# Kernel tuning notes

Hardware: AMD Instinct MI355X
Metric: run time of the kernel (lower is better)

## Reference

```python
import jax, jax.numpy as jnp
import numpy as np

V, E, H, L, B, T = 32000, 512, 512, 2, 16, 128


def setup_inputs() -> dict:
    key = jax.random.key(0)
    ks = jax.random.split(key, 12)
    s = 0.05  # small init to keep gates in a sane range
    return {
        "embedding": jax.random.normal(ks[0], (V, E), jnp.float32),
        "h": jax.random.normal(ks[1], (L, B, H), jnp.float32),
        "c": jax.random.normal(ks[2], (L, B, H), jnp.float32),
        "encoder_outputs": jax.random.normal(ks[3], (T, B, H), jnp.float32),
        # LSTM layer 0: input_size = H + E
        "w_ih0": jax.random.normal(ks[4], (4 * H, H + E), jnp.float32) * s,
        "w_hh0": jax.random.normal(ks[5], (4 * H, H), jnp.float32) * s,
        "b_ih0": jnp.zeros((4 * H,), jnp.float32),
        "b_hh0": jnp.zeros((4 * H,), jnp.float32),
        # LSTM layer 1: input_size = H
        "w_ih1": jax.random.normal(ks[6], (4 * H, H), jnp.float32) * s,
        "w_hh1": jax.random.normal(ks[7], (4 * H, H), jnp.float32) * s,
        "b_ih1": jnp.zeros((4 * H,), jnp.float32),
        "b_hh1": jnp.zeros((4 * H,), jnp.float32),
        # output projection to vocab
        "out_w": jax.random.normal(ks[8], (V, H), jnp.float32) * s,
        "out_b": jnp.zeros((V,), jnp.float32),
    }


def reference(embedding, h, c, encoder_outputs,
              w_ih0, w_hh0, b_ih0, b_hh0,
              w_ih1, w_hh1, b_ih1, b_hh1,
              out_w, out_b):
    T_, B_, _ = encoder_outputs.shape

    def cell(x, hp, cp, wi, wh, bi, bh):
        # PyTorch LSTM gate order: i, f, g, o
        g = x @ wi.T + hp @ wh.T + (bi + bh)
        i, f, gg, o = jnp.split(g, 4, axis=-1)
        cn = jax.nn.sigmoid(f) * cp + jax.nn.sigmoid(i) * jnp.tanh(gg)
        hn = jax.nn.sigmoid(o) * jnp.tanh(cn)
        return hn, cn

    def step(carry, _):
        tok, hs, cs = carry          # tok: [B] int, hs/cs: [L,B,H]
        emb = embedding[tok]         # [B,E] pretrained-embedding lookup
        # dot attention: query = top LSTM layer hidden state
        scores = jnp.einsum('bh,sbh->bs', hs[-1], encoder_outputs)
        aw = jax.nn.softmax(scores, axis=-1)               # [B,S]
        ctx = jnp.einsum('bs,sbh->bh', aw, encoder_outputs)  # [B,H]
        x = jnp.concatenate([emb, ctx], axis=-1)           # [B,E+H]
        h0, c0 = cell(x, hs[0], cs[0], w_ih0, w_hh0, b_ih0, b_hh0)
        h1, c1 = cell(h0, hs[1], cs[1], w_ih1, w_hh1, b_ih1, b_hh1)
        logp = jax.nn.log_softmax(h1 @ out_w.T + out_b, axis=-1)  # [B,V]
        nxt = jnp.argmax(logp, axis=-1).astype(jnp.int32)  # greedy (topk(1))
        return (nxt, jnp.stack([h0, h1]), jnp.stack([c0, c1])), (logp, nxt, aw)

    tok0 = jnp.ones((B_,), jnp.int32)  # torch.ones(batch_size) start token
    _, (logp, seq, attn) = jax.lax.scan(step, (tok0, h, c), None, length=T_)
    # torch cats along dim=1 -> [B, T, ...]
    return (jnp.transpose(logp, (1, 0, 2)),
            jnp.transpose(seq, (1, 0)),
            jnp.transpose(attn, (1, 0, 2)))
```

## Files before the change

### kernel.cpp

```cpp
#include <hip/hip_runtime.h>
#include <math.h>

#define VV 32000
#define EE 512
#define HH 512
#define BB 16
#define TT 128
#define SS 128
#define XD 1024
#define NPB 500
#define VB 64
#define SROW 1728

__device__ __forceinline__ float sigf(float x) { return 1.0f / (1.0f + expf(-x)); }

__global__ __launch_bounds__(256) void k_proj(
    const float* __restrict__ out_w, const float* __restrict__ out_b,
    const float* __restrict__ h1,
    const float* __restrict__ enc,
    float* __restrict__ raw, long rawstride, int nt_raw,
    float* __restrict__ scores,
    float* __restrict__ pmax, float* __restrict__ psum, int* __restrict__ pidx,
    int npb, int do_scores)
{
    const int blk = blockIdx.x;
    const int tid = threadIdx.x;

    if (blk >= npb) {
        if (!do_scores) return;
        const int b = blk - npb;
        const int s = tid >> 1, h = tid & 1;
        const float* er = enc + ((long)s * BB + b) * HH + h * 256;
        const float* hh = h1 + b * HH + h * 256;
        float acc = 0.f;
        #pragma unroll 8
        for (int k = 0; k < 256; k += 4) {
            float4 w = *(const float4*)(er + k);
            float4 x = *(const float4*)(hh + k);
            acc += w.x * x.x + w.y * x.y + w.z * x.z + w.w * x.w;
        }
        acc += __shfl_xor(acc, 1);
        if (h == 0) scores[b * SS + s] = acc;
        return;
    }

    __shared__ float h1t[10304];
    __shared__ float lv[64][17];

    for (int i = tid; i < BB * HH; i += 256) {
        int b = i >> 9, k = i & 511;
        h1t[k * 20 + ((k >> 6) << 2) + b] = h1[i];
    }
    __syncthreads();

    const int q = tid >> 3;
    const int h = tid & 7;
    const int v = blk * VB + q * 2;
    const float* w0 = out_w + (long)v * HH;
    const float* w1 = w0 + HH;
    float acc0[16], acc1[16];
    #pragma unroll
    for (int i = 0; i < 16; ++i) { acc0[i] = 0.f; acc1[i] = 0.f; }

    const int kbase = h * 64;
    for (int kk = 0; kk < 64; kk += 4) {
        const int k = kbase + kk;
        float a0f[4], a1f[4];
        *(float4*)a0f = *(const float4*)(w0 + k);
        *(float4*)a1f = *(const float4*)(w1 + k);
        #pragma unroll
        for (int d = 0; d < 4; ++d) {
            const int kd = k + d;
            const float* hp = &h1t[kd * 20 + ((kd >> 6) << 2)];
            const float wA = a0f[d], wB = a1f[d];
            #pragma unroll
            for (int g = 0; g < 4; ++g) {
                float hvf[4];
                *(float4*)hvf = *(const float4*)(hp + g * 4);
                acc0[g*4+0] += wA * hvf[0]; acc0[g*4+1] += wA * hvf[1];
                acc0[g*4+2] += wA * hvf[2]; acc0[g*4+3] += wA * hvf[3];
                acc1[g*4+0] += wB * hvf[0]; acc1[g*4+1] += wB * hvf[1];
                acc1[g*4+2] += wB * hvf[2]; acc1[g*4+3] += wB * hvf[3];
            }
        }
    }
    #pragma unroll
    for (int i = 0; i < 16; ++i) {
        float a = acc0[i];
        a += __shfl_xor(a, 1); a += __shfl_xor(a, 2); a += __shfl_xor(a, 4);
        acc0[i] = a;
        float c = acc1[i];
        c += __shfl_xor(c, 1); c += __shfl_xor(c, 2); c += __shfl_xor(c, 4);
        acc1[i] = c;
    }
    if (h == 0) {
        const float b0 = out_b[v], b1 = out_b[v + 1];
        #pragma unroll
        for (int b = 0; b < 16; ++b) {
            const float l0 = acc0[b] + b0, l1 = acc1[b] + b1;
            lv[q * 2][b] = l0; lv[q * 2 + 1][b] = l1;
            float* dst = raw + (long)b * rawstride + v;
            if (nt_raw) {
                __builtin_nontemporal_store(l0, dst);
                __builtin_nontemporal_store(l1, dst + 1);
            } else {
                dst[0] = l0; dst[1] = l1;
            }
        }
    }
    __syncthreads();

    const int b2 = tid >> 4;
    const int l  = tid & 15;
    float vals[4];
    float m = -INFINITY; int mi = 0;
    #pragma unroll
    for (int r = 0; r < 4; ++r) {
        const float x = lv[l * 4 + r][b2];
        vals[r] = x;
        if (x > m) { m = x; mi = l * 4 + r; }
    }
    #pragma unroll
    for (int off = 8; off >= 1; off >>= 1) {
        const float om = __shfl_xor(m, off);
        const int   oi = __shfl_xor(mi, off);
        if (om > m || (om == m && oi < mi)) { m = om; mi = oi; }
    }
    float z = 0.f;
    #pragma unroll
    for (int r = 0; r < 4; ++r) z += expf(vals[r] - m);
    #pragma unroll
    for (int off = 8; off >= 1; off >>= 1) z += __shfl_xor(z, off);
    if (l == 0) {
        pmax[blk * 16 + b2] = m;
        psum[blk * 16 + b2] = z;
        pidx[blk * 16 + b2] = blk * VB + mi;
    }
}

__global__ __launch_bounds__(256) void k_prep(
    const float* __restrict__ embedding,
    const float* __restrict__ enc,
    const float* __restrict__ scores,
    const float* __restrict__ raw, long rawstride, int nt_raw,
    const float* __restrict__ pmax, const float* __restrict__ psum, const int* __restrict__ pidx,
    float* __restrict__ xout,
    float* __restrict__ logp_out, float* __restrict__ seq_out, float* __restrict__ attn_out,
    int t, int mode, int npb)
{
    const int b = blockIdx.x >> 4;
    const int chunk = blockIdx.x & 15;
    const int tid = threadIdx.x;

    __shared__ float sm[256]; __shared__ int si[256]; __shared__ float ssum[256];
    __shared__ float aw[SS];  __shared__ float sred[2];

    int tok = 1;
    if (mode & 1) {
        float m = -INFINITY; int mi = 0x7fffffff;
        for (int i = tid; i < npb; i += 256) {
            const float pm = pmax[i * 16 + b];
            const int   pi = pidx[i * 16 + b];
            if (pm > m || (pm == m && pi < mi)) { m = pm; mi = pi; }
        }
        sm[tid] = m; si[tid] = mi;
        __syncthreads();
        for (int o = 128; o > 0; o >>= 1) {
            if (tid < o) {
                const float om = sm[tid + o]; const int oi = si[tid + o];
                if (om > sm[tid] || (om == sm[tid] && oi < si[tid])) { sm[tid] = om; si[tid] = oi; }
            }
            __syncthreads();
        }
        const float M = sm[0]; tok = si[0];
        float z = 0.f;
        for (int i = tid; i < npb; i += 256)
            z += psum[i * 16 + b] * expf(pmax[i * 16 + b] - M);
        ssum[tid] = z;
        __syncthreads();
        for (int o = 128; o > 0; o >>= 1) {
            if (tid < o) ssum[tid] += ssum[tid + o];
            __syncthreads();
        }
        const float lse = M + logf(ssum[0]);

        const float* rb = raw + (long)b * rawstride + chunk * 2000;
        float* ob = logp_out + ((long)b * TT + (t - 1)) * VV + chunk * 2000;
        if (nt_raw) {
            for (int i = tid; i < 2000; i += 256)
                __builtin_nontemporal_store(__builtin_nontemporal_load(rb + i) - lse, ob + i);
        } else {
            for (int i = tid; i < 2000; i += 256)
                __builtin_nontemporal_store(rb[i] - lse, ob + i);
        }
        if (chunk == 0 && tid == 0)
            __builtin_nontemporal_store((float)tok, seq_out + b * TT + (t - 1));
    }
    if (!(mode & 2)) return;
    __syncthreads();

    if (tid == 0) {
        float mm = -INFINITY;
        for (int s = 0; s < SS; ++s) mm = fmaxf(mm, scores[b * SS + s]);
        sred[0] = mm;
    }
    __syncthreads();
    if (tid < SS) aw[tid] = expf(scores[b * SS + tid] - sred[0]);
    __syncthreads();
    if (tid == 0) {
        float sum = 0.f;
        for (int s = 0; s < SS; ++s) sum += aw[s];
        sred[1] = 1.0f / sum;
    }
    __syncthreads();
    if (tid < SS) aw[tid] *= sred[1];
    __syncthreads();
    if (chunk == 0 && tid < SS)
        __builtin_nontemporal_store(aw[tid], attn_out + ((long)b * TT + t) * SS + tid);

    const int e0 = chunk * 64;
    if (e0 < EE) {
        for (int i = tid; i < 64; i += 256)
            xout[b * XD + e0 + i] = embedding[(long)tok * EE + e0 + i];
    } else {
        const int h0 = e0 - EE;
        __shared__ float ps[4][64];
        const int o = tid & 63, part = tid >> 6;
        float a = 0.f;
        for (int s2 = part * 32; s2 < part * 32 + 32; ++s2)
            a += aw[s2] * enc[((long)s2 * BB + b) * HH + h0 + o];
        ps[part][o] = a;
        __syncthreads();
        if (tid < 64)
            xout[b * XD + e0 + tid] = ps[0][tid] + ps[1][tid] + ps[2][tid] + ps[3][tid];
    }
}

__global__ __launch_bounds__(256) void k_lstm(
    const float* __restrict__ wih, const float* __restrict__ whh,
    const float* __restrict__ bih, const float* __restrict__ bhh,
    const float* __restrict__ xin, int xlen, int xshift,
    const float* __restrict__ hprev, const float* __restrict__ cprev,
    float* __restrict__ hout, float* __restrict__ cout)
{
    __shared__ float xs[BB * SROW];
    __shared__ float gpart[8 * 16 * 17];

    const int tid = threadIdx.x;
    const int j0 = blockIdx.x * 2;
    const int tot = xlen + HH;

    const int xmask = xlen - 1;
    for (int i = tid; i < (BB << xshift); i += 256) {
        const int b = i >> xshift, k = i & xmask;
        xs[b * SROW + k + ((k >> 5) << 2)] = xin[i];
    }
    for (int i = tid; i < BB * HH; i += 256) {
        const int b = i >> 9, k = xlen + (i & 511);
        xs[b * SROW + k + ((k >> 5) << 2)] = hprev[i];
    }
    __syncthreads();

    const int b = tid >> 4;
    const int h = tid & 15;
    const int klen = tot >> 4;
    const int k0 = h * klen;

    const float* pih[8]; const float* phh[8];
    #pragma unroll
    for (int r = 0; r < 8; ++r) {
        const int g = r >> 1, jj = r & 1;
        const int row = g * HH + j0 + jj;
        pih[r] = wih + (long)row * xlen;
        phh[r] = whh + (long)row * HH - xlen;
    }
    float acc[8];
    #pragma unroll
    for (int r = 0; r < 8; ++r) acc[r] = 0.f;

    const float* xb = xs + b * SROW;
    #pragma unroll 4
    for (int i = 0; i < klen; i += 4) {
        const int k = k0 + i;
        float xvf[4];
        *(float4*)xvf = *(const float4*)(xb + k + ((k >> 5) << 2));
        #pragma unroll
        for (int r = 0; r < 8; ++r) {
            const float* wp = ((k < xlen) ? pih[r] : phh[r]) + k;
            float wvf[4];
            *(float4*)wvf = *(const float4*)wp;
            acc[r] += wvf[0]*xvf[0] + wvf[1]*xvf[1] + wvf[2]*xvf[2] + wvf[3]*xvf[3];
        }
    }
    #pragma unroll
    for (int r = 0; r < 8; ++r) gpart[(r * 16 + b) * 17 + h] = acc[r];
    __syncthreads();

    if (tid < 128) {
        const int r = tid >> 4, bb = tid & 15;
        float s = 0.f;
        #pragma unroll
        for (int hh2 = 0; hh2 < 16; ++hh2) s += gpart[(r * 16 + bb) * 17 + hh2];
        const int g = r >> 1, jj = r & 1;
        const int row = g * HH + j0 + jj;
        gpart[(r * 16 + bb) * 17 + 16] = s + bih[row] + bhh[row];
    }
    __syncthreads();

    if (tid < 32) {
        const int bb = tid >> 1, jj = tid & 1;
        const float ii = gpart[((0 + jj) * 16 + bb) * 17 + 16];
        const float ff = gpart[((2 + jj) * 16 + bb) * 17 + 16];
        const float gg = gpart[((4 + jj) * 16 + bb) * 17 + 16];
        const float oo = gpart[((6 + jj) * 16 + bb) * 17 + 16];
        const int j = j0 + jj;
        const float cp = cprev[bb * HH + j];
        const float cn = sigf(ff) * cp + sigf(ii) * tanhf(gg);
        const float hn = sigf(oo) * tanhf(cn);
        hout[bb * HH + j] = hn;
        cout[bb * HH + j] = cn;
    }
}

extern "C" void kernel_launch(void* const* d_in, const int* in_sizes, int n_in,
                              void* d_out, int out_size, void* d_ws, size_t ws_size,
                              hipStream_t stream)
{
    (void)in_sizes; (void)n_in; (void)out_size;

    const float* embedding = (const float*)d_in[0];
    const float* h_in  = (const float*)d_in[1];
    const float* c_in  = (const float*)d_in[2];
    const float* enc   = (const float*)d_in[3];
    const float* w_ih0 = (const float*)d_in[4];
    const float* w_hh0 = (const float*)d_in[5];
    const float* b_ih0 = (const float*)d_in[6];
    const float* b_hh0 = (const float*)d_in[7];
    const float* w_ih1 = (const float*)d_in[8];
    const float* w_hh1 = (const float*)d_in[9];
    const float* b_ih1 = (const float*)d_in[10];
    const float* b_hh1 = (const float*)d_in[11];
    const float* out_w = (const float*)d_in[12];
    const float* out_b = (const float*)d_in[13];

    float* out = (float*)d_out;
    const long logp_sz = (long)BB * TT * VV;
    const long seq_sz  = (long)BB * TT;
    float* seq_out  = out + logp_sz;
    float* attn_out = out + logp_sz + seq_sz;

    float* ws = (float*)d_ws;
    const int BH = BB * HH;
    float* st     = ws;
    float* xbuf   = st + 8 * BH;
    float* scores = xbuf + BB * XD;
    float* pm     = scores + BB * SS;
    float* psm    = pm + NPB * BB;
    int*   pid    = (int*)(psm + NPB * BB);
    float* lraw   = (float*)(pid + NPB * BB);
    const size_t need = (size_t)((char*)(lraw + (long)BB * VV) - (char*)ws);
    const int usews = (ws_size >= need) ? 1 : 0;
    const int nt_raw = usews ? 0 : 1;
    const long rawstride = usews ? (long)VV : (long)TT * VV;

    auto sbuf = [&](int buf, int slot) { return st + (size_t)(buf * 4 + slot) * BH; };

    k_proj<<<16, 256, 0, stream>>>(out_w, out_b, h_in + BH, enc,
                                   usews ? lraw : out, rawstride, nt_raw,
                                   scores, pm, psm, pid, 0, 1);

    for (int t = 0; t <= TT; ++t) {
        const int mode = (t > 0 ? 1 : 0) | (t < TT ? 2 : 0);
        const float* rawprev = usews ? lraw : out + (size_t)(t > 0 ? t - 1 : 0) * VV;
        k_prep<<<256, 256, 0, stream>>>(embedding, enc, scores,
                                        rawprev, rawstride, nt_raw,
                                        pm, psm, pid, xbuf,
                                        out, seq_out, attn_out, t, mode, NPB);
        if (t == TT) break;

        const float* h0c = t ? sbuf(t & 1, 0) : h_in;
        const float* c0c = t ? sbuf(t & 1, 1) : c_in;
        const float* h1c = t ? sbuf(t & 1, 2) : h_in + BH;
        const float* c1c = t ? sbuf(t & 1, 3) : c_in + BH;
        const int n = (t + 1) & 1;
        float* h0n = sbuf(n, 0); float* c0n = sbuf(n, 1);
        float* h1n = sbuf(n, 2); float* c1n = sbuf(n, 3);

        k_lstm<<<256, 256, 0, stream>>>(w_ih0, w_hh0, b_ih0, b_hh0,
                                        xbuf, 1024, 10, h0c, c0c, h0n, c0n);
        k_lstm<<<256, 256, 0, stream>>>(w_ih1, w_hh1, b_ih1, b_hh1,
                                        h0n, 512, 9, h1c, c1c, h1n, c1n);

        float* rawt = usews ? lraw : out + (size_t)t * VV;
        k_proj<<<NPB + 16, 256, 0, stream>>>(out_w, out_b, h1n, enc,
                                             rawt, rawstride, nt_raw,
                                             scores, pm, psm, pid, NPB, 1);
    }
}
```

Before: 13.02 ms.

## Fuse decode loop into one persistent cooperative kernel with grid syncs

Replaces the per-timestep launches of prep, two LSTM and projection kernels with a single cooperative kernel that loops over all timesteps and separates stages with grid-wide syncs. The vocab projection is retiled to 128 rows per 512-thread block with a register reduce-scatter, and the attention, context and log-softmax finalisation stages are redistributed across blocks. The aim is to remove hundreds of kernel launch gaps and the per-launch reload of small state. In exchange it depends on cooperative launch residency (256 blocks of 512 threads) and pays the latency of four grid barriers per step.

```diff
diff --git a/kernel.cpp b/kernel.cpp
--- a/kernel.cpp
+++ b/kernel.cpp
@@ -1,5 +1,8 @@
 #include <hip/hip_runtime.h>
+#include <hip/hip_cooperative_groups.h>
 #include <math.h>
+
+namespace cg = cooperative_groups;
 
 #define VV 32000
 #define EE 512
@@ -8,317 +11,347 @@
 #define TT 128
 #define SS 128
 #define XD 1024
-#define NPB 500
-#define VB 64
-#define SROW 1728
-
-__device__ __forceinline__ float sigf(float x) { return 1.0f / (1.0f + expf(-x)); }
-
-__global__ __launch_bounds__(256) void k_proj(
-    const float* __restrict__ out_w, const float* __restrict__ out_b,
-    const float* __restrict__ h1,
-    const float* __restrict__ enc,
-    float* __restrict__ raw, long rawstride, int nt_raw,
-    float* __restrict__ scores,
-    float* __restrict__ pmax, float* __restrict__ psum, int* __restrict__ pidx,
-    int npb, int do_scores)
-{
+#define NPB 250
+#define BH (BB*HH)
+
+__device__ __forceinline__ float sigf(float x){ return 1.0f/(1.0f+expf(-x)); }
+
+__device__ __forceinline__ float fget(const float4& v, int d){
+    return d==0 ? v.x : d==1 ? v.y : d==2 ? v.z : v.w;
+}
+
+__device__ __forceinline__ int lvoff(int row){ return row * 20 + (((row >> 2) & 1) << 2); }
+
+__device__ __forceinline__ float bredmax(float v, float* s8, int tid){
+    #pragma unroll
+    for (int o = 32; o >= 1; o >>= 1) v = fmaxf(v, __shfl_xor(v, o));
+    if ((tid & 63) == 0) s8[tid >> 6] = v;
+    __syncthreads();
+    float r = fmaxf(fmaxf(fmaxf(s8[0],s8[1]),fmaxf(s8[2],s8[3])),
+                    fmaxf(fmaxf(s8[4],s8[5]),fmaxf(s8[6],s8[7])));
+    __syncthreads();
+    return r;
+}
+__device__ __forceinline__ float bredsum(float v, float* s8, int tid){
+    #pragma unroll
+    for (int o = 32; o >= 1; o >>= 1) v += __shfl_xor(v, o);
+    if ((tid & 63) == 0) s8[tid >> 6] = v;
+    __syncthreads();
+    float r = ((s8[0]+s8[1])+(s8[2]+s8[3]))+((s8[4]+s8[5])+(s8[6]+s8[7]));
+    __syncthreads();
+    return r;
+}
+__device__ __forceinline__ void bredamax(float& v, int& idx, float* s8, int* si8, int tid){
+    #pragma unroll
+    for (int o = 32; o >= 1; o >>= 1){
+        float ov = __shfl_xor(v, o); int oi = __shfl_xor(idx, o);
+        if (ov > v || (ov == v && oi < idx)) { v = ov; idx = oi; }
+    }
+    if ((tid & 63) == 0) { s8[tid >> 6] = v; si8[tid >> 6] = idx; }
+    __syncthreads();
+    float bv = s8[0]; int bi = si8[0];
+    #pragma unroll
+    for (int w = 1; w < 8; ++w){
+        float ov = s8[w]; int oi = si8[w];
+        if (ov > bv || (ov == bv && oi < bi)) { bv = ov; bi = oi; }
+    }
+    __syncthreads();
+    v = bv; idx = bi;
+}
+
+template<int XLEN>
+__device__ __forceinline__ void lstm_cell(
+    int tid, int j0,
+    const float* __restrict__ wih, const float* __restrict__ whh,
+    const float* __restrict__ bih, const float* __restrict__ bhh,
+    const float* __restrict__ xsrc,
+    const float* __restrict__ hold, const float* __restrict__ cold,
+    float* __restrict__ hnew, float* __restrict__ cnew)
+{
+    const int bb = tid >> 5, h32 = tid & 31;
+    constexpr int KX = XLEN >> 5;
+    constexpr int KH = 16;
+    float acc[8];
+    #pragma unroll
+    for (int r = 0; r < 8; ++r) acc[r] = 0.f;
+    const float* xb = xsrc + bb * XLEN + h32 * KX;
+    const float* hb = hold + (bb << 9) + h32 * KH;
+    const float* wx[8]; const float* wh[8];
+    #pragma unroll
+    for (int r = 0; r < 8; ++r) {
+        const int row = (r >> 1) * HH + j0 + (r & 1);
+        wx[r] = wih + (long)row * XLEN + h32 * KX;
+        wh[r] = whh + ((long)row << 9) + h32 * KH;
+    }
+    #pragma unroll
+    for (int i = 0; i < KX; i += 4) {
+        float4 xv = *(const float4*)(xb + i);
+        #pragma unroll
+        for (int r = 0; r < 8; ++r) {
+            float4 wv = *(const float4*)(wx[r] + i);
+            acc[r] = fmaf(wv.w, xv.w, fmaf(wv.z, xv.z, fmaf(wv.y, xv.y, fmaf(wv.x, xv.x, acc[r]))));
+        }
+    }
+    #pragma unroll
+    for (int i = 0; i < KH; i += 4) {
+        float4 xv = *(const float4*)(hb + i);
+        #pragma unroll
+        for (int r = 0; r < 8; ++r) {
+            float4 wv = *(const float4*)(wh[r] + i);
+            acc[r] = fmaf(wv.w, xv.w, fmaf(wv.z, xv.z, fmaf(wv.y, xv.y, fmaf(wv.x, xv.x, acc[r]))));
+        }
+    }
+    #pragma unroll
+    for (int o = 16; o >= 1; o >>= 1) {
+        #pragma unroll
+        for (int r = 0; r < 8; ++r) acc[r] += __shfl_xor(acc[r], o);
+    }
+    if (h32 == 0) {
+        #pragma unroll
+        for (int jj = 0; jj < 2; ++jj) {
+            const int j = j0 + jj;
+            const float gi = acc[0 + jj] + bih[j]          + bhh[j];
+            const float gf = acc[2 + jj] + bih[HH + j]     + bhh[HH + j];
+            const float gg = acc[4 + jj] + bih[2*HH + j]   + bhh[2*HH + j];
+            const float go = acc[6 + jj] + bih[3*HH + j]   + bhh[3*HH + j];
+            const float cp = cold[(bb << 9) + j];
+            const float cn = sigf(gf) * cp + sigf(gi) * tanhf(gg);
+            const float hn = sigf(go) * tanhf(cn);
+            hnew[(bb << 9) + j] = hn;
+            cnew[(bb << 9) + j] = cn;
+        }
+    }
+}
+
+__device__ __forceinline__ void calc_scores(int blk, int tid,
+    const float* __restrict__ h1, const float* __restrict__ enc, float* __restrict__ scores)
+{
+    const int idx = (blk - NPB) * 512 + tid;
+    if (idx >= BB * SS) return;
+    const int s = idx >> 4, b = idx & 15;
+    const float* ep = enc + ((long)s * BB + b) * HH;
+    const float* hp = h1 + b * HH;
+    float a0 = 0.f, a1 = 0.f, a2 = 0.f, a3 = 0.f;
+    #pragma unroll 2
+    for (int k = 0; k < HH; k += 16) {
+        float4 e0 = *(const float4*)(ep + k),      hv0 = *(const float4*)(hp + k);
+        float4 e1 = *(const float4*)(ep + k + 4),  hv1 = *(const float4*)(hp + k + 4);
+        float4 e2 = *(const float4*)(ep + k + 8),  hv2 = *(const float4*)(hp + k + 8);
+        float4 e3 = *(const float4*)(ep + k + 12), hv3 = *(const float4*)(hp + k + 12);
+        a0 += e0.x*hv0.x + e0.y*hv0.y + e0.z*hv0.z + e0.w*hv0.w;
+        a1 += e1.x*hv1.x + e1.y*hv1.y + e1.z*hv1.z + e1.w*hv1.w;
+        a2 += e2.x*hv2.x + e2.y*hv2.y + e2.z*hv2.z + e2.w*hv2.w;
+        a3 += e3.x*hv3.x + e3.y*hv3.y + e3.z*hv3.z + e3.w*hv3.w;
+    }
+    scores[b * SS + s] = (a0 + a1) + (a2 + a3);
+}
+
+__device__ __forceinline__ void proj_tile(
+    int blk, int tid, const float* __restrict__ h1,
+    const float* __restrict__ ow, const float* __restrict__ ob,
+    float* __restrict__ rawt, long rstride,
+    float* __restrict__ pm, float* __restrict__ psm, int* __restrict__ pid,
+    float* __restrict__ h1t, float* __restrict__ lv)
+{
+    for (int i = tid; i < BB * HH; i += 512) {
+        const int b = i >> 9, k = i & 511;
+        h1t[k * 20 + ((k >> 5) << 2) + b] = h1[i];
+    }
+    __syncthreads();
+
+    const int q = tid >> 4, h = tid & 15;
+    const int v0 = blk * 128 + q * 4;
+    const int k0 = h << 5;
+    float a[64];
+    #pragma unroll
+    for (int i = 0; i < 64; ++i) a[i] = 0.f;
+
+    const float* w0 = ow + (long)v0 * HH + k0;
+    #pragma unroll 2
+    for (int kk = 0; kk < 32; kk += 4) {
+        float4 wv0 = *(const float4*)(w0 + kk);
+        float4 wv1 = *(const float4*)(w0 + HH + kk);
+        float4 wv2 = *(const float4*)(w0 + 2 * HH + kk);
+        float4 wv3 = *(const float4*)(w0 + 3 * HH + kk);
+        #pragma unroll
+        for (int d = 0; d < 4; ++d) {
+            const int kd = k0 + kk + d;
+            const float* hp = h1t + kd * 20 + ((kd >> 5) << 2);
+            float4 hv0 = *(const float4*)(hp);
+            float4 hv1 = *(const float4*)(hp + 4);
+            float4 hv2 = *(const float4*)(hp + 8);
+            float4 hv3 = *(const float4*)(hp + 12);
+            const float hv[16] = {hv0.x,hv0.y,hv0.z,hv0.w, hv1.x,hv1.y,hv1.z,hv1.w,
+                                  hv2.x,hv2.y,hv2.z,hv2.w, hv3.x,hv3.y,hv3.z,hv3.w};
+            const float wr[4] = { fget(wv0,d), fget(wv1,d), fget(wv2,d), fget(wv3,d) };
+            #pragma unroll
+            for (int r = 0; r < 4; ++r)
+                #pragma unroll
+                for (int j = 0; j < 16; ++j)
+                    a[r*16+j] = fmaf(wr[r], hv[j], a[r*16+j]);
+        }
+    }
+
+#define RS_ROUND(O, NH)                                                  \
+    {                                                                    \
+        const bool up = (h & (O)) != 0;                                  \
+        _Pragma("unroll")                                                \
+        for (int i = 0; i < (NH); ++i) {                                 \
+            float lo = a[i], hi = a[i + (NH)];                           \
+            float snd = up ? lo : hi;                                    \
+            float rcv = __shfl_xor(snd, (O));                            \
+            a[i] = (up ? hi : lo) + rcv;                                 \
+        }                                                                \
+    }
+    RS_ROUND(1, 32)
+    RS_ROUND(2, 16)
+    RS_ROUND(4, 8)
+    RS_ROUND(8, 4)
+#undef RS_ROUND
+    const int br = ((h & 1) << 3) | ((h & 2) << 1) | ((h & 4) >> 1) | ((h & 8) >> 3);
+    const int rr = br >> 2;
+    const int jb = (br & 3) << 2;
+    {
+        const int row = q * 4 + rr;
+        const float bv = ob[v0 + rr];
+        float* dst = lv + lvoff(row) + jb;
+        float4 val = { a[0] + bv, a[1] + bv, a[2] + bv, a[3] + bv };
+        *(float4*)dst = val;
+    }
+    __syncthreads();
+
+    for (int i = tid; i < 128 * BB; i += 512) {
+        const int b = i >> 7, row = i & 127;
+        rawt[(long)b * rstride + blk * 128 + row] = lv[lvoff(row) + b];
+    }
+
+    const int b2 = tid >> 5, l = tid & 31;
+    float vals[4]; float m = -INFINITY; int mi = 0;
+    #pragma unroll
+    for (int r = 0; r < 4; ++r) {
+        const int row = l * 4 + r;
+        const float x = lv[lvoff(row) + b2];
+        vals[r] = x;
+        if (x > m) { m = x; mi = row; }
+    }
+    #pragma unroll
+    for (int o = 16; o >= 1; o >>= 1) {
+        float om = __shfl_xor(m, o); int oi = __shfl_xor(mi, o);
+        if (om > m || (om == m && oi < mi)) { m = om; mi = oi; }
+    }
+    float z = 0.f;
+    #pragma unroll
+    for (int r = 0; r < 4; ++r) z += expf(vals[r] - m);
+    #pragma unroll
+    for (int o = 16; o >= 1; o >>= 1) z += __shfl_xor(z, o);
+    if (l == 0) {
+        pm[blk * BB + b2] = m;
+        psm[blk * BB + b2] = z;
+        pid[blk * BB + b2] = blk * 128 + mi;
+    }
+}
+
+struct Params {
+    const float *emb, *h0i, *c0i, *enc;
+    const float *wih0, *whh0, *bih0, *bhh0;
+    const float *wih1, *whh1, *bih1, *bhh1;
+    const float *ow, *ob;
+    float *out, *seqo, *attn;
+    float *st, *xbuf, *scores, *pm, *psm;
+    int *pid;
+    float *lraw;
+    int usews;
+};
+
+__global__ __launch_bounds__(512, 2) void k_decode(Params p)
+{
+    cg::grid_group grid = cg::this_grid();
     const int blk = blockIdx.x;
     const int tid = threadIdx.x;
 
-    if (blk >= npb) {
-        if (!do_scores) return;
-        const int b = blk - npb;
-        const int s = tid >> 1, h = tid & 1;
-        const float* er = enc + ((long)s * BB + b) * HH + h * 256;
-        const float* hh = h1 + b * HH + h * 256;
-        float acc = 0.f;
-        #pragma unroll 8
-        for (int k = 0; k < 256; k += 4) {
-            float4 w = *(const float4*)(er + k);
-            float4 x = *(const float4*)(hh + k);
-            acc += w.x * x.x + w.y * x.y + w.z * x.z + w.w * x.w;
-        }
-        acc += __shfl_xor(acc, 1);
-        if (h == 0) scores[b * SS + s] = acc;
-        return;
-    }
-
-    __shared__ float h1t[10304];
-    __shared__ float lv[64][17];
-
-    for (int i = tid; i < BB * HH; i += 256) {
-        int b = i >> 9, k = i & 511;
-        h1t[k * 20 + ((k >> 6) << 2) + b] = h1[i];
-    }
-    __syncthreads();
-
-    const int q = tid >> 3;
-    const int h = tid & 7;
-    const int v = blk * VB + q * 2;
-    const float* w0 = out_w + (long)v * HH;
-    const float* w1 = w0 + HH;
-    float acc0[16], acc1[16];
-    #pragma unroll
-    for (int i = 0; i < 16; ++i) { acc0[i] = 0.f; acc1[i] = 0.f; }
-
-    const int kbase = h * 64;
-    for (int kk = 0; kk < 64; kk += 4) {
-        const int k = kbase + kk;
-        float a0f[4], a1f[4];
-        *(float4*)a0f = *(const float4*)(w0 + k);
-        *(float4*)a1f = *(const float4*)(w1 + k);
-        #pragma unroll
-        for (int d = 0; d < 4; ++d) {
-            const int kd = k + d;
-            const float* hp = &h1t[kd * 20 + ((kd >> 6) << 2)];
-            const float wA = a0f[d], wB = a1f[d];
-            #pragma unroll
-            for (int g = 0; g < 4; ++g) {
-                float hvf[4];
-                *(float4*)hvf = *(const float4*)(hp + g * 4);
-                acc0[g*4+0] += wA * hvf[0]; acc0[g*4+1] += wA * hvf[1];
-                acc0[g*4+2] += wA * hvf[2]; acc0[g*4+3] += wA * hvf[3];
-                acc1[g*4+0] += wB * hvf[0]; acc1[g*4+1] += wB * hvf[1];
-                acc1[g*4+2] += wB * hvf[2]; acc1[g*4+3] += wB * hvf[3];
+    __shared__ float smem[12896];
+    float* h1t = smem;
+    float* lv  = smem + 10304;
+    float* aw  = smem;
+    float* s8  = smem + 160;
+    int*   si8 = (int*)(smem + 176);
+
+    if (blk >= NPB) calc_scores(blk, tid, p.h0i + BH, p.enc, p.scores);
+    grid.sync();
+
+    for (int t = 0; t <= TT; ++t) {
+        if (blk < BB) {
+            const int b = blk;
+            int tok = 1;
+            if (t > 0) {
+                float m = -INFINITY; int mi = 0x7fffffff;
+                if (tid < NPB) { m = p.pm[tid * BB + b]; mi = p.pid[tid * BB + b]; }
+                bredamax(m, mi, s8, si8, tid);
+                tok = mi;
+                if (tid == 0) p.seqo[b * TT + (t - 1)] = (float)tok;
             }
-        }
-    }
-    #pragma unroll
-    for (int i = 0; i < 16; ++i) {
-        float a = acc0[i];
-        a += __shfl_xor(a, 1); a += __shfl_xor(a, 2); a += __shfl_xor(a, 4);
-        acc0[i] = a;
-        float c = acc1[i];
-        c += __shfl_xor(c, 1); c += __shfl_xor(c, 2); c += __shfl_xor(c, 4);
-        acc1[i] = c;
-    }
-    if (h == 0) {
-        const float b0 = out_b[v], b1 = out_b[v + 1];
-        #pragma unroll
-        for (int b = 0; b < 16; ++b) {
-            const float l0 = acc0[b] + b0, l1 = acc1[b] + b1;
-            lv[q * 2][b] = l0; lv[q * 2 + 1][b] = l1;
-            float* dst = raw + (long)b * rawstride + v;
-            if (nt_raw) {
-                __builtin_nontemporal_store(l0, dst);
-                __builtin_nontemporal_store(l1, dst + 1);
-            } else {
-                dst[0] = l0; dst[1] = l1;
+            if (t < TT) {
+                float sc = (tid < SS) ? p.scores[b * SS + tid] : -INFINITY;
+                float M = bredmax(sc, s8, tid);
+                float e = (tid < SS) ? expf(sc - M) : 0.f;
+                float Z = bredsum(e, s8, tid);
+                float av = e / Z;
+                if (tid < SS) {
+                    aw[tid] = av;
+                    __builtin_nontemporal_store(av, p.attn + ((long)b * TT + t) * SS + tid);
+                }
+                __syncthreads();
+                float cacc = 0.f;
+                const float* ep = p.enc + b * HH + tid;
+                #pragma unroll 8
+                for (int s = 0; s < SS; ++s)
+                    cacc = fmaf(aw[s], ep[(long)s * BH], cacc);
+                p.xbuf[b * XD + EE + tid] = cacc;
+                p.xbuf[b * XD + tid] = p.emb[(long)tok * EE + tid];
             }
-        }
-    }
-    __syncthreads();
-
-    const int b2 = tid >> 4;
-    const int l  = tid & 15;
-    float vals[4];
-    float m = -INFINITY; int mi = 0;
-    #pragma unroll
-    for (int r = 0; r < 4; ++r) {
-        const float x = lv[l * 4 + r][b2];
-        vals[r] = x;
-        if (x > m) { m = x; mi = l * 4 + r; }
-    }
-    #pragma unroll
-    for (int off = 8; off >= 1; off >>= 1) {
-        const float om = __shfl_xor(m, off);
-        const int   oi = __shfl_xor(mi, off);
-        if (om > m || (om == m && oi < mi)) { m = om; mi = oi; }
-    }
-    float z = 0.f;
-    #pragma unroll
-    for (int r = 0; r < 4; ++r) z += expf(vals[r] - m);
-    #pragma unroll
-    for (int off = 8; off >= 1; off >>= 1) z += __shfl_xor(z, off);
-    if (l == 0) {
-        pmax[blk * 16 + b2] = m;
-        psum[blk * 16 + b2] = z;
-        pidx[blk * 16 + b2] = blk * VB + mi;
-    }
-}
-
-__global__ __launch_bounds__(256) void k_prep(
-    const float* __restrict__ embedding,
-    const float* __restrict__ enc,
-    const float* __restrict__ scores,
-    const float* __restrict__ raw, long rawstride, int nt_raw,
-    const float* __restrict__ pmax, const float* __restrict__ psum, const int* __restrict__ pidx,
-    float* __restrict__ xout,
-    float* __restrict__ logp_out, float* __restrict__ seq_out, float* __restrict__ attn_out,
-    int t, int mode, int npb)
-{
-    const int b = blockIdx.x >> 4;
-    const int chunk = blockIdx.x & 15;
-    const int tid = threadIdx.x;
-
-    __shared__ float sm[256]; __shared__ int si[256]; __shared__ float ssum[256];
-    __shared__ float aw[SS];  __shared__ float sred[2];
-
-    int tok = 1;
-    if (mode & 1) {
-        float m = -INFINITY; int mi = 0x7fffffff;
-        for (int i = tid; i < npb; i += 256) {
-            const float pm = pmax[i * 16 + b];
-            const int   pi = pidx[i * 16 + b];
-            if (pm > m || (pm == m && pi < mi)) { m = pm; mi = pi; }
-        }
-        sm[tid] = m; si[tid] = mi;
-        __syncthreads();
-        for (int o = 128; o > 0; o >>= 1) {
-            if (tid < o) {
-                const float om = sm[tid + o]; const int oi = si[tid + o];
-                if (om > sm[tid] || (om == sm[tid] && oi < si[tid])) { sm[tid] = om; si[tid] = oi; }
-            }
-            __syncthreads();
-        }
-        const float M = sm[0]; tok = si[0];
-        float z = 0.f;
-        for (int i = tid; i < npb; i += 256)
-            z += psum[i * 16 + b] * expf(pmax[i * 16 + b] - M);
-        ssum[tid] = z;
-        __syncthreads();
-        for (int o = 128; o > 0; o >>= 1) {
-            if (tid < o) ssum[tid] += ssum[tid + o];
-            __syncthreads();
-        }
-        const float lse = M + logf(ssum[0]);
-
-        const float* rb = raw + (long)b * rawstride + chunk * 2000;
-        float* ob = logp_out + ((long)b * TT + (t - 1)) * VV + chunk * 2000;
-        if (nt_raw) {
-            for (int i = tid; i < 2000; i += 256)
-                __builtin_nontemporal_store(__builtin_nontemporal_load(rb + i) - lse, ob + i);
-        } else {
-            for (int i = tid; i < 2000; i += 256)
-                __builtin_nontemporal_store(rb[i] - lse, ob + i);
-        }
-        if (chunk == 0 && tid == 0)
-            __builtin_nontemporal_store((float)tok, seq_out + b * TT + (t - 1));
-    }
-    if (!(mode & 2)) return;
-    __syncthreads();
-
-    if (tid == 0) {
-        float mm = -INFINITY;
-        for (int s = 0; s < SS; ++s) mm = fmaxf(mm, scores[b * SS + s]);
-        sred[0] = mm;
-    }
-    __syncthreads();
-    if (tid < SS) aw[tid] = expf(scores[b * SS + tid] - sred[0]);
-    __syncthreads();
-    if (tid == 0) {
-        float sum = 0.f;
-        for (int s = 0; s < SS; ++s) sum += aw[s];
-        sred[1] = 1.0f / sum;
-    }
-    __syncthreads();
-    if (tid < SS) aw[tid] *= sred[1];
-    __syncthreads();
-    if (chunk == 0 && tid < SS)
-        __builtin_nontemporal_store(aw[tid], attn_out + ((long)b * TT + t) * SS + tid);
-
-    const int e0 = chunk * 64;
-    if (e0 < EE) {
-        for (int i = tid; i < 64; i += 256)
-            xout[b * XD + e0 + i] = embedding[(long)tok * EE + e0 + i];
-    } else {
-        const int h0 = e0 - EE;
-        __shared__ float ps[4][64];
-        const int o = tid & 63, part = tid >> 6;
-        float a = 0.f;
-        for (int s2 = part * 32; s2 < part * 32 + 32; ++s2)
-            a += aw[s2] * enc[((long)s2 * BB + b) * HH + h0 + o];
-        ps[part][o] = a;
-        __syncthreads();
-        if (tid < 64)
-            xout[b * XD + e0 + tid] = ps[0][tid] + ps[1][tid] + ps[2][tid] + ps[3][tid];
-    }
-}
-
-__global__ __launch_bounds__(256) void k_lstm(
-    const float* __restrict__ wih, const float* __restrict__ whh,
-    const float* __restrict__ bih, const float* __restrict__ bhh,
-    const float* __restrict__ xin, int xlen, int xshift,
-    const float* __restrict__ hprev, const float* __restrict__ cprev,
-    float* __restrict__ hout, float* __restrict__ cout)
-{
-    __shared__ float xs[BB * SROW];
-    __shared__ float gpart[8 * 16 * 17];
-
-    const int tid = threadIdx.x;
-    const int j0 = blockIdx.x * 2;
-    const int tot = xlen + HH;
-
-    const int xmask = xlen - 1;
-    for (int i = tid; i < (BB << xshift); i += 256) {
-        const int b = i >> xshift, k = i & xmask;
-        xs[b * SROW + k + ((k >> 5) << 2)] = xin[i];
-    }
-    for (int i = tid; i < BB * HH; i += 256) {
-        const int b = i >> 9, k = xlen + (i & 511);
-        xs[b * SROW + k + ((k >> 5) << 2)] = hprev[i];
-    }
-    __syncthreads();
-
-    const int b = tid >> 4;
-    const int h = tid & 15;
-    const int klen = tot >> 4;
-    const int k0 = h * klen;
-
-    const float* pih[8]; const float* phh[8];
-    #pragma unroll
-    for (int r = 0; r < 8; ++r) {
-        const int g = r >> 1, jj = r & 1;
-        const int row = g * HH + j0 + jj;
-        pih[r] = wih + (long)row * xlen;
-        phh[r] = whh + (long)row * HH - xlen;
-    }
-    float acc[8];
-    #pragma unroll
-    for (int r = 0; r < 8; ++r) acc[r] = 0.f;
-
-    const float* xb = xs + b * SROW;
-    #pragma unroll 4
-    for (int i = 0; i < klen; i += 4) {
-        const int k = k0 + i;
-        float xvf[4];
-        *(float4*)xvf = *(const float4*)(xb + k + ((k >> 5) << 2));
-        #pragma unroll
-        for (int r = 0; r < 8; ++r) {
-            const float* wp = ((k < xlen) ? pih[r] : phh[r]) + k;
-            float wvf[4];
-            *(float4*)wvf = *(const float4*)wp;
-            acc[r] += wvf[0]*xvf[0] + wvf[1]*xvf[1] + wvf[2]*xvf[2] + wvf[3]*xvf[3];
-        }
-    }
-    #pragma unroll
-    for (int r = 0; r < 8; ++r) gpart[(r * 16 + b) * 17 + h] = acc[r];
-    __syncthreads();
-
-    if (tid < 128) {
-        const int r = tid >> 4, bb = tid & 15;
-        float s = 0.f;
-        #pragma unroll
-        for (int hh2 = 0; hh2 < 16; ++hh2) s += gpart[(r * 16 + bb) * 17 + hh2];
-        const int g = r >> 1, jj = r & 1;
-        const int row = g * HH + j0 + jj;
-        gpart[(r * 16 + bb) * 17 + 16] = s + bih[row] + bhh[row];
-    }
-    __syncthreads();
-
-    if (tid < 32) {
-        const int bb = tid >> 1, jj = tid & 1;
-        const float ii = gpart[((0 + jj) * 16 + bb) * 17 + 16];
-        const float ff = gpart[((2 + jj) * 16 + bb) * 17 + 16];
-        const float gg = gpart[((4 + jj) * 16 + bb) * 17 + 16];
-        const float oo = gpart[((6 + jj) * 16 + bb) * 17 + 16];
-        const int j = j0 + jj;
-        const float cp = cprev[bb * HH + j];
-        const float cn = sigf(ff) * cp + sigf(ii) * tanhf(gg);
-        const float hn = sigf(oo) * tanhf(cn);
-        hout[bb * HH + j] = hn;
-        cout[bb * HH + j] = cn;
+        } else if (t > 0) {
+            const int wb = blk - BB;
+            const int b = wb / 15, c = wb - b * 15;
+            float m = (tid < NPB) ? p.pm[tid * BB + b] : -INFINITY;
+            m = bredmax(m, s8, tid);
+            float z = (tid < NPB) ? p.psm[tid * BB + b] * expf(p.pm[tid * BB + b] - m) : 0.f;
+            z = bredsum(z, s8, tid);
+            const float lse = m + logf(z);
+            const long obase = ((long)b * TT + (t - 1)) * (long)VV;
+            const float* rb = p.usews ? (p.lraw + (long)b * VV) : (p.out + obase);
+            float* obp = p.out + obase;
+            const int v0 = c * 2134, v1 = min(v0 + 2134, VV);
+            for (int v = v0 + tid; v < v1; v += 512)
+                __builtin_nontemporal_store(__builtin_nontemporal_load(rb + v) - lse, obp + v);
+        }
+        if (t == TT) return;
+        grid.sync();
+
+        const int po = t & 1, pn = (t + 1) & 1;
+        const float* h0o = t ? p.st + (po * 4 + 0) * BH : p.h0i;
+        const float* c0o = t ? p.st + (po * 4 + 1) * BH : p.c0i;
+        const float* h1o = t ? p.st + (po * 4 + 2) * BH : p.h0i + BH;
+        const float* c1o = t ? p.st + (po * 4 + 3) * BH : p.c0i + BH;
+        float* h0n = p.st + (pn * 4 + 0) * BH;
+        float* c0n = p.st + (pn * 4 + 1) * BH;
+        float* h1n = p.st + (pn * 4 + 2) * BH;
+        float* c1n = p.st + (pn * 4 + 3) * BH;
+
+        lstm_cell<XD>(tid, blk * 2, p.wih0, p.whh0, p.bih0, p.bhh0, p.xbuf, h0o, c0o, h0n, c0n);
+        grid.sync();
+
+        lstm_cell<HH>(tid, blk * 2, p.wih1, p.whh1, p.bih1, p.bhh1, h0n, h1o, c1o, h1n, c1n);
+        grid.sync();
+
+        {
+            float* rawt = p.usews ? p.lraw : p.out + (long)t * VV;
+            const long rstride = p.usews ? (long)VV : (long)TT * (long)VV;
+            if (blk < NPB)
+                proj_tile(blk, tid, h1n, p.ow, p.ob, rawt, rstride, p.pm, p.psm, p.pid, h1t, lv);
+            else
+                calc_scores(blk, tid, h1n, p.enc, p.scores);
+        }
+        grid.sync();
     }
 }
 
@@ -327,73 +360,38 @@
                               hipStream_t stream)
 {
     (void)in_sizes; (void)n_in; (void)out_size;
-
-    const float* embedding = (const float*)d_in[0];
-    const float* h_in  = (const float*)d_in[1];
-    const float* c_in  = (const float*)d_in[2];
-    const float* enc   = (const float*)d_in[3];
-    const float* w_ih0 = (const float*)d_in[4];
-    const float* w_hh0 = (const float*)d_in[5];
-    const float* b_ih0 = (const float*)d_in[6];
-    const float* b_hh0 = (const float*)d_in[7];
-    const float* w_ih1 = (const float*)d_in[8];
-    const float* w_hh1 = (const float*)d_in[9];
-    const float* b_ih1 = (const float*)d_in[10];
-    const float* b_hh1 = (const float*)d_in[11];
-    const float* out_w = (const float*)d_in[12];
-    const float* out_b = (const float*)d_in[13];
+    Params p;
+    p.emb  = (const float*)d_in[0];
+    p.h0i  = (const float*)d_in[1];
+    p.c0i  = (const float*)d_in[2];
+    p.enc  = (const float*)d_in[3];
+    p.wih0 = (const float*)d_in[4];
+    p.whh0 = (const float*)d_in[5];
+    p.bih0 = (const float*)d_in[6];
+    p.bhh0 = (const float*)d_in[7];
+    p.wih1 = (const float*)d_in[8];
+    p.whh1 = (const float*)d_in[9];
+    p.bih1 = (const float*)d_in[10];
+    p.bhh1 = (const float*)d_in[11];
+    p.ow   = (const float*)d_in[12];
+    p.ob   = (const float*)d_in[13];
 
     float* out = (float*)d_out;
-    const long logp_sz = (long)BB * TT * VV;
-    const long seq_sz  = (long)BB * TT;
-    float* seq_out  = out + logp_sz;
-    float* attn_out = out + logp_sz + seq_sz;
+    p.out  = out;
+    p.seqo = out + (long)BB * TT * VV;
+    p.attn = p.seqo + (long)BB * TT;
 
     float* ws = (float*)d_ws;
-    const int BH = BB * HH;
-    float* st     = ws;
-    float* xbuf   = st + 8 * BH;
-    float* scores = xbuf + BB * XD;
-    float* pm     = scores + BB * SS;
-    float* psm    = pm + NPB * BB;
-    int*   pid    = (int*)(psm + NPB * BB);
-    float* lraw   = (float*)(pid + NPB * BB);
-    const size_t need = (size_t)((char*)(lraw + (long)BB * VV) - (char*)ws);
-    const int usews = (ws_size >= need) ? 1 : 0;
-    const int nt_raw = usews ? 0 : 1;
-    const long rawstride = usews ? (long)VV : (long)TT * VV;
-
-    auto sbuf = [&](int buf, int slot) { return st + (size_t)(buf * 4 + slot) * BH; };
-
-    k_proj<<<16, 256, 0, stream>>>(out_w, out_b, h_in + BH, enc,
-                                   usews ? lraw : out, rawstride, nt_raw,
-                                   scores, pm, psm, pid, 0, 1);
-
-    for (int t = 0; t <= TT; ++t) {
-        const int mode = (t > 0 ? 1 : 0) | (t < TT ? 2 : 0);
-        const float* rawprev = usews ? lraw : out + (size_t)(t > 0 ? t - 1 : 0) * VV;
-        k_prep<<<256, 256, 0, stream>>>(embedding, enc, scores,
-                                        rawprev, rawstride, nt_raw,
-                                        pm, psm, pid, xbuf,
-                                        out, seq_out, attn_out, t, mode, NPB);
-        if (t == TT) break;
-
-        const float* h0c = t ? sbuf(t & 1, 0) : h_in;
-        const float* c0c = t ? sbuf(t & 1, 1) : c_in;
-        const float* h1c = t ? sbuf(t & 1, 2) : h_in + BH;
-        const float* c1c = t ? sbuf(t & 1, 3) : c_in + BH;
-        const int n = (t + 1) & 1;
-        float* h0n = sbuf(n, 0); float* c0n = sbuf(n, 1);
-        float* h1n = sbuf(n, 2); float* c1n = sbuf(n, 3);
-
-        k_lstm<<<256, 256, 0, stream>>>(w_ih0, w_hh0, b_ih0, b_hh0,
-                                        xbuf, 1024, 10, h0c, c0c, h0n, c0n);
-        k_lstm<<<256, 256, 0, stream>>>(w_ih1, w_hh1, b_ih1, b_hh1,
-                                        h0n, 512, 9, h1c, c1c, h1n, c1n);
-
-        float* rawt = usews ? lraw : out + (size_t)t * VV;
-        k_proj<<<NPB + 16, 256, 0, stream>>>(out_w, out_b, h1n, enc,
-                                             rawt, rawstride, nt_raw,
-                                             scores, pm, psm, pid, NPB, 1);
-    }
-}
+    p.st     = ws;
+    p.xbuf   = p.st + 8 * BH;
+    p.scores = p.xbuf + BB * XD;
+    p.pm     = p.scores + BB * SS;
+    p.psm    = p.pm + NPB * BB;
+    p.pid    = (int*)(p.psm + NPB * BB);
+    p.lraw   = (float*)(p.pid + NPB * BB);
+    const size_t need = (size_t)((char*)(p.lraw + (long)BB * VV) - (char*)ws);
+    p.usews = (ws_size >= need) ? 1 : 0;
+
+    void* args[] = { &p };
+    hipLaunchCooperativeKernel((void*)k_decode, dim3(256), dim3(512), args, 0, stream);
+}
```

Result: slower. 28.53 ms, median of 2 (+119.1%).
